# Kernel tuning notes

Hardware: AMD Instinct MI355X
Metric: run time of the kernel (lower is better)

The kernel has to match this reference:

```python
import jax, jax.numpy as jnp
import numpy as np

B, C, H, W = 8, 256, 64, 64
DQK = 16  # int(sqrt(out_channels))


def setup_inputs() -> dict:
    key = jax.random.key(0)
    ks = jax.random.split(key, 8)
    s_in = 1.0 / np.sqrt(C)
    return {
        "x": jax.random.normal(ks[0], (B, C, H, W), dtype=jnp.float32),
        "Wf": jax.random.normal(ks[1], (DQK, C), dtype=jnp.float32) * s_in,
        "bf": jnp.zeros((DQK,), dtype=jnp.float32),
        "Wg": jax.random.normal(ks[2], (DQK, C), dtype=jnp.float32) * s_in,
        "bg": jnp.zeros((DQK,), dtype=jnp.float32),
        "Wh": jax.random.normal(ks[3], (C, C), dtype=jnp.float32) * s_in,
        "bh": jnp.zeros((C,), dtype=jnp.float32),
        # original inits attention_multiplier to 0.0; use small nonzero so output depends on attention path
        "gamma": jnp.float32(0.5),
    }


def reference(x, Wf, bf, Wg, bg, Wh, bh, gamma):
    b, c, h, w = x.shape
    hw = h * w
    # 1x1 convs == per-pixel channel projections
    f = (jnp.einsum('bchw,oc->bohw', x, Wf) + bf[None, :, None, None]).reshape(b, -1, hw)  # [B,DQK,HW]
    g = (jnp.einsum('bchw,oc->bohw', x, Wg) + bg[None, :, None, None]).reshape(b, -1, hw)  # [B,DQK,HW]
    hh = (jnp.einsum('bchw,oc->bohw', x, Wh) + bh[None, :, None, None]).reshape(b, -1, hw)  # [B,C,HW]
    # s[b,n,m] = sum_k g[b,k,n] * f[b,k,m]  -> [B,HW,HW]
    s = jnp.einsum('bkn,bkm->bnm', g, f)
    beta = jax.nn.softmax(s, axis=-1)
    # o = beta @ h^T, then transpose back to channel-first: [B,C,HW]
    o = jnp.einsum('bnm,bcm->bcn', beta, hh)
    return gamma * o.reshape(x.shape) + x
```

## Files before the change

### kernel.cpp

```cpp
#include <hip/hip_runtime.h>
#include <math.h>

#define BATCH 8
#define CH    256
#define HWN   4096
#define DQK   16

typedef __attribute__((ext_vector_type(8))) short short8;
typedef __attribute__((ext_vector_type(4))) float float4v;

__device__ __forceinline__ unsigned short f2bf(float f) {
    union { float f; unsigned int u; } v; v.f = f;
    unsigned int r = v.u + 0x7FFF + ((v.u >> 16) & 1);
    return (unsigned short)(r >> 16);
}
__device__ __forceinline__ unsigned int cvtpk(float lo, float hi) {
    unsigned int r;
    asm("v_cvt_pk_bf16_f32 %0, %1, %2" : "=v"(r) : "v"(lo), "v"(hi));
    return r;
}
__device__ __forceinline__ int perm_ft(int m) {
    return (m & ~28) | ((m & 24) >> 1) | ((m & 4) << 2);
}

__global__ __launch_bounds__(256) void wcast_kernel(
    const float* __restrict__ Wf, const float* __restrict__ bf_,
    const float* __restrict__ Wg, const float* __restrict__ bg,
    const float* __restrict__ Wh, const float* __restrict__ bh,
    unsigned short* __restrict__ Wbf, float* __restrict__ bcat)
{
    const int r = blockIdx.x;
    const int t = threadIdx.x;
    const float* src = (r < 16) ? (Wf + r*CH) : (r < 32) ? (Wg + (r-16)*CH) : (Wh + (r-32)*CH);
    Wbf[r*CH + t] = f2bf(src[t]);
    if (t == 0) bcat[r] = (r < 16) ? bf_[r] : (r < 32) ? bg[r-16] : bh[r-32];
}

__global__ __launch_bounds__(256) void xt_kernel(const float* __restrict__ x,
                                                 unsigned short* __restrict__ xt)
{
    const int t  = threadIdx.x;
    const int p0 = blockIdx.x * 64;
    const int c0 = blockIdx.y * 64;
    const int b  = blockIdx.z;
    __shared__ unsigned short tile[64][73];
    const int pc = t & 63;
    const int r0 = (t >> 6) * 16;
    #pragma unroll
    for (int j = 0; j < 16; j++) {
        int c = r0 + j;
        tile[pc][c] = f2bf(x[(size_t)(b*CH + c0 + c)*HWN + p0 + pc]);
    }
    __syncthreads();
    const int pr = t >> 2;
    const int cb = (t & 3) * 16;
    unsigned int outv[8];
    #pragma unroll
    for (int i = 0; i < 8; i++)
        outv[i] = (unsigned int)tile[pr][cb + 2*i] | ((unsigned int)tile[pr][cb + 2*i + 1] << 16);
    unsigned short* dst = &xt[(size_t)(b*HWN + p0 + pr)*CH + c0 + cb];
    *(uint4*)dst       = *(uint4*)&outv[0];
    *(uint4*)(dst + 8) = *(uint4*)&outv[4];
}

__global__ __launch_bounds__(256, 6) void proj_kernel(
    const unsigned short* __restrict__ xt, const unsigned short* __restrict__ Wbf,
    const float* __restrict__ bcat,
    unsigned short* __restrict__ ft, unsigned short* __restrict__ g,
    unsigned short* __restrict__ h3)
{
    const int t      = threadIdx.x;
    const int px0    = blockIdx.x * 64;
    const int b      = blockIdx.y;
    const int rtbase = blockIdx.z * 6;
    const int lane = t & 63, w = t >> 6, l15 = lane & 15, quad = lane >> 4;

    float4v acc[6];
    #pragma unroll
    for (int rt = 0; rt < 6; rt++) acc[rt] = (float4v){0.f,0.f,0.f,0.f};

    const unsigned short* xrow = &xt[((size_t)(b*HWN + px0 + w*16 + l15))*CH + quad*8];
    const unsigned short* wrow = &Wbf[(size_t)l15*CH + quad*8];

    #pragma unroll
    for (int ks = 0; ks < 8; ks++) {
        short8 afrag = *(const short8*)&xrow[ks*32];
        #pragma unroll
        for (int rt = 0; rt < 6; rt++) {
            short8 bfrag = *(const short8*)&wrow[(size_t)(rtbase + rt)*16*CH + ks*32];
            acc[rt] = __builtin_amdgcn_mfma_f32_16x16x32_bf16(afrag, bfrag, acc[rt], 0, 0, 0);
        }
    }

    const int pxl = px0 + w*16 + quad*4;
    const int mt  = (px0 >> 5) + (w >> 1);
    const int sub = ((w & 1)*2 + (quad >> 1))*128 + l15*8 + (quad & 1)*4;
    #pragma unroll
    for (int rt = 0; rt < 6; rt++) {
        const int R = rtbase + rt;
        if (R == 0) {
            float bv = bcat[l15];
            const int s0 = perm_ft(pxl);
            unsigned int p01 = cvtpk(acc[rt][0] + bv, acc[rt][1] + bv);
            unsigned int p23 = cvtpk(acc[rt][2] + bv, acc[rt][3] + bv);
            unsigned short* fp0 = &ft[((size_t)b*HWN + s0)*32];
            fp0[l15]       = (unsigned short)p01;         fp0[16 + l15]  = 0;
            fp0[32 + l15]  = (unsigned short)(p01 >> 16); fp0[48 + l15]  = 0;
            fp0[64 + l15]  = (unsigned short)p23;         fp0[80 + l15]  = 0;
            fp0[96 + l15]  = (unsigned short)(p23 >> 16); fp0[112 + l15] = 0;
        } else if (R == 1) {
            float bv = bcat[16 + l15];
            unsigned int a01 = cvtpk(acc[rt][0] + bv, acc[rt][1] + bv);
            unsigned int a23 = cvtpk(acc[rt][2] + bv, acc[rt][3] + bv);
            *(uint2*)&g[(size_t)(b*DQK + l15)*HWN + pxl] = make_uint2(a01, a23);
        } else {
            float bv = bcat[R*16 + l15];
            unsigned int u0 = cvtpk(acc[rt][0] + bv, acc[rt][1] + bv);
            unsigned int u1 = cvtpk(acc[rt][2] + bv, acc[rt][3] + bv);
            *(uint2*)&h3[(((size_t)((b*128 + mt)*16 + (R-2))) << 9) + sub] = make_uint2(u0, u1);
        }
    }
}

__global__ __launch_bounds__(512, 4) void attn_kernel(
    const unsigned short* __restrict__ ft, const unsigned short* __restrict__ g,
    const unsigned short* __restrict__ h3, const float* __restrict__ x,
    const float* __restrict__ gamma_p, float* __restrict__ out)
{
    const int t    = threadIdx.x;
    const int b    = blockIdx.x & 7;
    const int q0   = (blockIdx.x >> 3) * 64;
    const int lane = t & 63, w = t >> 6, l15 = lane & 15, quad = lane >> 4;
    const int qt_w = w >> 1, half = w & 1;

    __shared__ __align__(16) uint4 pB[2][2][4][64];
    __shared__ float l_l[4][16][2];

    union { short8 v; unsigned short u[8]; } gfrag;
    #pragma unroll
    for (int j = 0; j < 8; j++) {
        int k = quad*8 + j;
        gfrag.u[j] = (k < DQK) ? g[(size_t)(b*DQK + k)*HWN + q0 + qt_w*16 + l15] : (unsigned short)0;
    }

    const unsigned short* ftb = ft + (size_t)b*HWN*32;
    const unsigned short* h3b = h3 + ((size_t)b << 20);

    short8 fr[2][2], hr[2][2][2];
    float4v acc[2][4];
    #pragma unroll
    for (int i = 0; i < 2; i++)
        #pragma unroll
        for (int j = 0; j < 4; j++) acc[i][j] = (float4v){0.f,0.f,0.f,0.f};
    float l_acc = 0.f;
    uint4 P;

    #pragma unroll
    for (int j = 0; j < 2; j++)
        fr[0][j] = *(const short8*)&ftb[(size_t)((half*2 + j)*16 + l15)*32 + quad*8];
    {
        float4v z = {0.f,0.f,0.f,0.f};
        float4v s0v = __builtin_amdgcn_mfma_f32_16x16x32_bf16(fr[0][0], gfrag.v, z, 0, 0, 0);
        float4v s1v = __builtin_amdgcn_mfma_f32_16x16x32_bf16(fr[0][1], gfrag.v, z, 0, 0, 0);
        float e0 = __expf(s0v[0]), e1 = __expf(s0v[1]), e2 = __expf(s0v[2]), e3 = __expf(s0v[3]);
        float e4 = __expf(s1v[0]), e5 = __expf(s1v[1]), e6 = __expf(s1v[2]), e7 = __expf(s1v[3]);
        l_acc += (e0 + e1) + (e2 + e3) + (e4 + e5) + (e6 + e7);
        P = make_uint4(cvtpk(e0, e1), cvtpk(e2, e3), cvtpk(e4, e5), cvtpk(e6, e7));
    }
    #pragma unroll
    for (int j = 0; j < 2; j++)
        fr[1][j] = *(const short8*)&ftb[(size_t)(64 + (half*2 + j)*16 + l15)*32 + quad*8];
    #pragma unroll
    for (int grp = 0; grp < 2; grp++)
        #pragma unroll
        for (int ctl = 0; ctl < 2; ctl++)
            hr[0][grp][ctl] = *(const short8*)&h3b[(((size_t)(grp*16 + w*2 + ctl)) << 9) + lane*8];

#define ATTN_STEP(u, i, DO_NEXT) do {                                          \
    pB[u][half][qt_w][lane] = P;                                               \
    __syncthreads();                                                           \
    if (DO_NEXT) {                                                             \
      const int nf = ((i) + 2) & 63;                                           \
      _Pragma("unroll")                                                        \
      for (int j = 0; j < 2; j++)                                              \
        fr[u][j] = *(const short8*)&ftb[(size_t)(nf*64 + (half*2 + j)*16 + l15)*32 + quad*8]; \
      const int nh = ((i) + 1) & 63;                                           \
      _Pragma("unroll")                                                        \
      for (int grp = 0; grp < 2; grp++)                                        \
        _Pragma("unroll")                                                      \
        for (int ctl = 0; ctl < 2; ctl++)                                      \
          hr[(u)^1][grp][ctl] = *(const short8*)&h3b[(((size_t)((nh*2 + grp)*16 + w*2 + ctl)) << 9) + lane*8]; \
      float4v z = {0.f,0.f,0.f,0.f};                                           \
      float4v s0v = __builtin_amdgcn_mfma_f32_16x16x32_bf16(fr[(u)^1][0], gfrag.v, z, 0, 0, 0); \
      float4v s1v = __builtin_amdgcn_mfma_f32_16x16x32_bf16(fr[(u)^1][1], gfrag.v, z, 0, 0, 0); \
      float e0 = __expf(s0v[0]), e1 = __expf(s0v[1]), e2 = __expf(s0v[2]), e3 = __expf(s0v[3]); \
      float e4 = __expf(s1v[0]), e5 = __expf(s1v[1]), e6 = __expf(s1v[2]), e7 = __expf(s1v[3]); \
      l_acc += (e0 + e1) + (e2 + e3) + (e4 + e5) + (e6 + e7);                  \
      P = make_uint4(cvtpk(e0, e1), cvtpk(e2, e3), cvtpk(e4, e5), cvtpk(e6, e7)); \
    }                                                                          \
    _Pragma("unroll")                                                          \
    for (int grp = 0; grp < 2; grp++) {                                        \
      _Pragma("unroll")                                                        \
      for (int qt = 0; qt < 4; qt++) {                                         \
        union { uint4 uu; short8 v; } bq;                                      \
        bq.uu = pB[u][grp][qt][lane];                                          \
        _Pragma("unroll")                                                      \
        for (int ctl = 0; ctl < 2; ctl++)                                      \
          acc[ctl][qt] = __builtin_amdgcn_mfma_f32_16x16x32_bf16(hr[u][grp][ctl], bq.v, acc[ctl][qt], 0, 0, 0); \
      }                                                                        \
    }                                                                          \
  } while (0)

    for (int i0 = 0; i0 < 62; i0 += 2) {
        ATTN_STEP(0, i0, 1);
        ATTN_STEP(1, i0 + 1, 1);
    }
    ATTN_STEP(0, 62, 1);
    ATTN_STEP(1, 63, 0);
#undef ATTN_STEP

    l_acc += __shfl_xor(l_acc, 16, 64);
    l_acc += __shfl_xor(l_acc, 32, 64);
    if (quad == 0) l_l[qt_w][l15][half] = l_acc;
    __syncthreads();

    const float gamma = *gamma_p;
    float linv[4];
    #pragma unroll
    for (int qt = 0; qt < 4; qt++) linv[qt] = 1.f / (l_l[qt][l15][0] + l_l[qt][l15][1]);
    #pragma unroll
    for (int ctl = 0; ctl < 2; ctl++) {
        #pragma unroll
        for (int r = 0; r < 4; r++) {
            int c = w*32 + ctl*16 + quad*4 + r;
            size_t base = (size_t)(b*CH + c)*HWN + q0;
            #pragma unroll
            for (int qt = 0; qt < 4; qt++) {
                size_t o = base + qt*16 + l15;
                out[o] = gamma * acc[ctl][qt][r] * linv[qt] + x[o];
            }
        }
    }
}

extern "C" void kernel_launch(void* const* d_in, const int* in_sizes, int n_in,
                              void* d_out, int out_size, void* d_ws, size_t ws_size,
                              hipStream_t stream) {
    const float* x     = (const float*)d_in[0];
    const float* Wf    = (const float*)d_in[1];
    const float* bf_   = (const float*)d_in[2];
    const float* Wg    = (const float*)d_in[3];
    const float* bg    = (const float*)d_in[4];
    const float* Wh    = (const float*)d_in[5];
    const float* bh    = (const float*)d_in[6];
    const float* gamma = (const float*)d_in[7];
    float* out = (float*)d_out;

    unsigned short* xt   = (unsigned short*)d_ws;
    unsigned short* ftp  = xt  + (size_t)BATCH*HWN*CH;
    unsigned short* g    = ftp + (size_t)BATCH*HWN*32;
    unsigned short* h3   = g   + (size_t)BATCH*DQK*HWN;
    unsigned short* Wbf  = h3  + (size_t)BATCH*128*16*512;
    float*          bcat = (float*)(Wbf + 288*CH);

    wcast_kernel<<<dim3(288), 256, 0, stream>>>(Wf, bf_, Wg, bg, Wh, bh, Wbf, bcat);
    xt_kernel<<<dim3(HWN/64, CH/64, BATCH), 256, 0, stream>>>(x, xt);
    proj_kernel<<<dim3(HWN/64, BATCH, 3), 256, 0, stream>>>(xt, Wbf, bcat, ftp, g, h3);
    attn_kernel<<<dim3((HWN/64)*BATCH), 512, 0, stream>>>(ftp, g, h3, x, gamma, out);
}
```

Measured before the change: 217.3 us.

## Process two key tiles per barrier, fold log2e into f, vectorize x transpose

The attention loop now handles two 64-key tiles per synchronization step, with double-buffered P tiles in shared memory. This halves the number of __syncthreads calls, and h3 is loaded at the top of each step instead of being prefetched a step ahead. log2(e) is folded into the f projection so the softmax can use the hardware exp2 instruction instead of __expf. The MFMA block is wrapped in s_setprio. The x transpose kernel now uses float4 loads with packed bf16 conversion and 32-bit shared-memory reads. The risks are higher register and LDS pressure and h3 load latency that is no longer prefetched.

```diff
diff --git a/kernel.cpp b/kernel.cpp
--- a/kernel.cpp
+++ b/kernel.cpp
@@ -9,6 +9,8 @@
 typedef __attribute__((ext_vector_type(8))) short short8;
 typedef __attribute__((ext_vector_type(4))) float float4v;
 
+#define L2E 1.4426950408889634f
+
 __device__ __forceinline__ unsigned short f2bf(float f) {
     union { float f; unsigned int u; } v; v.f = f;
     unsigned int r = v.u + 0x7FFF + ((v.u >> 16) & 1);
@@ -18,6 +20,13 @@
     unsigned int r;
     asm("v_cvt_pk_bf16_f32 %0, %1, %2" : "=v"(r) : "v"(lo), "v"(hi));
     return r;
+}
+__device__ __forceinline__ float ex2(float x) {
+#if __has_builtin(__builtin_amdgcn_exp2f)
+    return __builtin_amdgcn_exp2f(x);
+#else
+    return exp2f(x);
+#endif
 }
 __device__ __forceinline__ int perm_ft(int m) {
     return (m & ~28) | ((m & 24) >> 1) | ((m & 4) << 2);
@@ -43,13 +52,18 @@
     const int p0 = blockIdx.x * 64;
     const int c0 = blockIdx.y * 64;
     const int b  = blockIdx.z;
-    __shared__ unsigned short tile[64][73];
-    const int pc = t & 63;
-    const int r0 = (t >> 6) * 16;
-    #pragma unroll
-    for (int j = 0; j < 16; j++) {
-        int c = r0 + j;
-        tile[pc][c] = f2bf(x[(size_t)(b*CH + c0 + c)*HWN + p0 + pc]);
+    __shared__ unsigned short tile[64][74];
+    const int col4 = (t & 15) * 4;
+    const int cr   = t >> 4;
+    #pragma unroll
+    for (int j = 0; j < 4; j++) {
+        int c = cr + j*16;
+        float4 v = *(const float4*)&x[(size_t)(b*CH + c0 + c)*HWN + p0 + col4];
+        unsigned int u01 = cvtpk(v.x, v.y), u23 = cvtpk(v.z, v.w);
+        tile[col4+0][c] = (unsigned short)u01;
+        tile[col4+1][c] = (unsigned short)(u01 >> 16);
+        tile[col4+2][c] = (unsigned short)u23;
+        tile[col4+3][c] = (unsigned short)(u23 >> 16);
     }
     __syncthreads();
     const int pr = t >> 2;
@@ -57,7 +71,7 @@
     unsigned int outv[8];
     #pragma unroll
     for (int i = 0; i < 8; i++)
-        outv[i] = (unsigned int)tile[pr][cb + 2*i] | ((unsigned int)tile[pr][cb + 2*i + 1] << 16);
+        outv[i] = *(const unsigned int*)&tile[pr][cb + 2*i];
     unsigned short* dst = &xt[(size_t)(b*HWN + p0 + pr)*CH + c0 + cb];
     *(uint4*)dst       = *(uint4*)&outv[0];
     *(uint4*)(dst + 8) = *(uint4*)&outv[4];
@@ -101,8 +115,8 @@
         if (R == 0) {
             float bv = bcat[l15];
             const int s0 = perm_ft(pxl);
-            unsigned int p01 = cvtpk(acc[rt][0] + bv, acc[rt][1] + bv);
-            unsigned int p23 = cvtpk(acc[rt][2] + bv, acc[rt][3] + bv);
+            unsigned int p01 = cvtpk((acc[rt][0] + bv)*L2E, (acc[rt][1] + bv)*L2E);
+            unsigned int p23 = cvtpk((acc[rt][2] + bv)*L2E, (acc[rt][3] + bv)*L2E);
             unsigned short* fp0 = &ft[((size_t)b*HWN + s0)*32];
             fp0[l15]       = (unsigned short)p01;         fp0[16 + l15]  = 0;
             fp0[32 + l15]  = (unsigned short)(p01 >> 16); fp0[48 + l15]  = 0;
@@ -133,7 +147,7 @@
     const int lane = t & 63, w = t >> 6, l15 = lane & 15, quad = lane >> 4;
     const int qt_w = w >> 1, half = w & 1;
 
-    __shared__ __align__(16) uint4 pB[2][2][4][64];
+    __shared__ __align__(16) uint4 pB[4][2][4][64];
     __shared__ float l_l[4][16][2];
 
     union { short8 v; unsigned short u[8]; } gfrag;
@@ -146,78 +160,92 @@
     const unsigned short* ftb = ft + (size_t)b*HWN*32;
     const unsigned short* h3b = h3 + ((size_t)b << 20);
 
-    short8 fr[2][2], hr[2][2][2];
+    short8 fr[2][4];
     float4v acc[2][4];
     #pragma unroll
     for (int i = 0; i < 2; i++)
         #pragma unroll
         for (int j = 0; j < 4; j++) acc[i][j] = (float4v){0.f,0.f,0.f,0.f};
     float l_acc = 0.f;
-    uint4 P;
-
-    #pragma unroll
-    for (int j = 0; j < 2; j++)
-        fr[0][j] = *(const short8*)&ftb[(size_t)((half*2 + j)*16 + l15)*32 + quad*8];
+    uint4 Pa, Pb;
+
+#define EXP2_PACK(sv0, sv1, Pout) do {                                         \
+      float e0 = ex2((sv0)[0]), e1 = ex2((sv0)[1]), e2 = ex2((sv0)[2]), e3 = ex2((sv0)[3]); \
+      float e4 = ex2((sv1)[0]), e5 = ex2((sv1)[1]), e6 = ex2((sv1)[2]), e7 = ex2((sv1)[3]); \
+      l_acc += ((e0 + e1) + (e2 + e3)) + ((e4 + e5) + (e6 + e7));              \
+      Pout = make_uint4(cvtpk(e0, e1), cvtpk(e2, e3), cvtpk(e4, e5), cvtpk(e6, e7)); \
+    } while (0)
+
     {
+        short8 f0[4];
+        #pragma unroll
+        for (int j = 0; j < 4; j++)
+            f0[j] = *(const short8*)&ftb[(size_t)((j>>1)*64 + (half*2 + (j&1))*16 + l15)*32 + quad*8];
         float4v z = {0.f,0.f,0.f,0.f};
-        float4v s0v = __builtin_amdgcn_mfma_f32_16x16x32_bf16(fr[0][0], gfrag.v, z, 0, 0, 0);
-        float4v s1v = __builtin_amdgcn_mfma_f32_16x16x32_bf16(fr[0][1], gfrag.v, z, 0, 0, 0);
-        float e0 = __expf(s0v[0]), e1 = __expf(s0v[1]), e2 = __expf(s0v[2]), e3 = __expf(s0v[3]);
-        float e4 = __expf(s1v[0]), e5 = __expf(s1v[1]), e6 = __expf(s1v[2]), e7 = __expf(s1v[3]);
-        l_acc += (e0 + e1) + (e2 + e3) + (e4 + e5) + (e6 + e7);
-        P = make_uint4(cvtpk(e0, e1), cvtpk(e2, e3), cvtpk(e4, e5), cvtpk(e6, e7));
-    }
-    #pragma unroll
-    for (int j = 0; j < 2; j++)
-        fr[1][j] = *(const short8*)&ftb[(size_t)(64 + (half*2 + j)*16 + l15)*32 + quad*8];
-    #pragma unroll
-    for (int grp = 0; grp < 2; grp++)
-        #pragma unroll
-        for (int ctl = 0; ctl < 2; ctl++)
-            hr[0][grp][ctl] = *(const short8*)&h3b[(((size_t)(grp*16 + w*2 + ctl)) << 9) + lane*8];
-
-#define ATTN_STEP(u, i, DO_NEXT) do {                                          \
-    pB[u][half][qt_w][lane] = P;                                               \
+        float4v s0 = __builtin_amdgcn_mfma_f32_16x16x32_bf16(f0[0], gfrag.v, z, 0, 0, 0);
+        float4v s1 = __builtin_amdgcn_mfma_f32_16x16x32_bf16(f0[1], gfrag.v, z, 0, 0, 0);
+        float4v s2 = __builtin_amdgcn_mfma_f32_16x16x32_bf16(f0[2], gfrag.v, z, 0, 0, 0);
+        float4v s3 = __builtin_amdgcn_mfma_f32_16x16x32_bf16(f0[3], gfrag.v, z, 0, 0, 0);
+        EXP2_PACK(s0, s1, Pa);
+        EXP2_PACK(s2, s3, Pb);
+    }
+    #pragma unroll
+    for (int j = 0; j < 4; j++)
+        fr[0][j] = *(const short8*)&ftb[(size_t)((2 + (j>>1))*64 + (half*2 + (j&1))*16 + l15)*32 + quad*8];
+
+#define SUPER(U, T, DO_NEXT) do {                                              \
+    pB[(U)*2 + 0][half][qt_w][lane] = Pa;                                      \
+    pB[(U)*2 + 1][half][qt_w][lane] = Pb;                                      \
     __syncthreads();                                                           \
+    short8 hra[2][2], hrb[2][2];                                               \
+    _Pragma("unroll")                                                          \
+    for (int grp = 0; grp < 2; grp++) {                                        \
+      _Pragma("unroll")                                                        \
+      for (int ctl = 0; ctl < 2; ctl++) {                                      \
+        hra[grp][ctl] = *(const short8*)&h3b[(((size_t)((4*(T) + grp)*16 + w*2 + ctl)) << 9) + lane*8]; \
+        hrb[grp][ctl] = *(const short8*)&h3b[(((size_t)((4*(T) + 2 + grp)*16 + w*2 + ctl)) << 9) + lane*8]; \
+      }                                                                        \
+    }                                                                          \
     if (DO_NEXT) {                                                             \
-      const int nf = ((i) + 2) & 63;                                           \
       _Pragma("unroll")                                                        \
-      for (int j = 0; j < 2; j++)                                              \
-        fr[u][j] = *(const short8*)&ftb[(size_t)(nf*64 + (half*2 + j)*16 + l15)*32 + quad*8]; \
-      const int nh = ((i) + 1) & 63;                                           \
-      _Pragma("unroll")                                                        \
-      for (int grp = 0; grp < 2; grp++)                                        \
-        _Pragma("unroll")                                                      \
-        for (int ctl = 0; ctl < 2; ctl++)                                      \
-          hr[(u)^1][grp][ctl] = *(const short8*)&h3b[(((size_t)((nh*2 + grp)*16 + w*2 + ctl)) << 9) + lane*8]; \
+      for (int j = 0; j < 4; j++) {                                            \
+        const int nt = (2*(T) + 4 + (j>>1)) & 63;                              \
+        fr[(U)^1][j] = *(const short8*)&ftb[(size_t)(nt*64 + (half*2 + (j&1))*16 + l15)*32 + quad*8]; \
+      }                                                                        \
       float4v z = {0.f,0.f,0.f,0.f};                                           \
-      float4v s0v = __builtin_amdgcn_mfma_f32_16x16x32_bf16(fr[(u)^1][0], gfrag.v, z, 0, 0, 0); \
-      float4v s1v = __builtin_amdgcn_mfma_f32_16x16x32_bf16(fr[(u)^1][1], gfrag.v, z, 0, 0, 0); \
-      float e0 = __expf(s0v[0]), e1 = __expf(s0v[1]), e2 = __expf(s0v[2]), e3 = __expf(s0v[3]); \
-      float e4 = __expf(s1v[0]), e5 = __expf(s1v[1]), e6 = __expf(s1v[2]), e7 = __expf(s1v[3]); \
-      l_acc += (e0 + e1) + (e2 + e3) + (e4 + e5) + (e6 + e7);                  \
-      P = make_uint4(cvtpk(e0, e1), cvtpk(e2, e3), cvtpk(e4, e5), cvtpk(e6, e7)); \
+      float4v s0 = __builtin_amdgcn_mfma_f32_16x16x32_bf16(fr[U][0], gfrag.v, z, 0, 0, 0); \
+      float4v s1 = __builtin_amdgcn_mfma_f32_16x16x32_bf16(fr[U][1], gfrag.v, z, 0, 0, 0); \
+      float4v s2 = __builtin_amdgcn_mfma_f32_16x16x32_bf16(fr[U][2], gfrag.v, z, 0, 0, 0); \
+      float4v s3 = __builtin_amdgcn_mfma_f32_16x16x32_bf16(fr[U][3], gfrag.v, z, 0, 0, 0); \
+      EXP2_PACK(s0, s1, Pa);                                                   \
+      EXP2_PACK(s2, s3, Pb);                                                   \
     }                                                                          \
+    __builtin_amdgcn_s_setprio(1);                                             \
     _Pragma("unroll")                                                          \
     for (int grp = 0; grp < 2; grp++) {                                        \
       _Pragma("unroll")                                                        \
       for (int qt = 0; qt < 4; qt++) {                                         \
-        union { uint4 uu; short8 v; } bq;                                      \
-        bq.uu = pB[u][grp][qt][lane];                                          \
+        union { uint4 uu; short8 v; } bqa, bqb;                                \
+        bqa.uu = pB[(U)*2 + 0][grp][qt][lane];                                 \
+        bqb.uu = pB[(U)*2 + 1][grp][qt][lane];                                 \
         _Pragma("unroll")                                                      \
-        for (int ctl = 0; ctl < 2; ctl++)                                      \
-          acc[ctl][qt] = __builtin_amdgcn_mfma_f32_16x16x32_bf16(hr[u][grp][ctl], bq.v, acc[ctl][qt], 0, 0, 0); \
+        for (int ctl = 0; ctl < 2; ctl++) {                                    \
+          acc[ctl][qt] = __builtin_amdgcn_mfma_f32_16x16x32_bf16(hra[grp][ctl], bqa.v, acc[ctl][qt], 0, 0, 0); \
+          acc[ctl][qt] = __builtin_amdgcn_mfma_f32_16x16x32_bf16(hrb[grp][ctl], bqb.v, acc[ctl][qt], 0, 0, 0); \
+        }                                                                      \
       }                                                                        \
     }                                                                          \
+    __builtin_amdgcn_s_setprio(0);                                             \
   } while (0)
 
-    for (int i0 = 0; i0 < 62; i0 += 2) {
-        ATTN_STEP(0, i0, 1);
-        ATTN_STEP(1, i0 + 1, 1);
-    }
-    ATTN_STEP(0, 62, 1);
-    ATTN_STEP(1, 63, 0);
-#undef ATTN_STEP
+    for (int T = 0; T < 30; T += 2) {
+        SUPER(0, T, 1);
+        SUPER(1, T + 1, 1);
+    }
+    SUPER(0, 30, 1);
+    SUPER(1, 31, 0);
+#undef SUPER
+#undef EXP2_PACK
 
     l_acc += __shfl_xor(l_acc, 16, 64);
     l_acc += __shfl_xor(l_acc, 32, 64);
```

Result: slower. 253.6 us (+16.7%).
